# Kernel optimization log

Hardware: AMD Instinct MI355X
Metric: run time of the kernel (lower is better)

Reference implementation:

```python
import jax, jax.numpy as jnp
import numpy as np

B, L, D = 32, 128, 48          # batch, time steps, features
R = 64                          # no_reference_time_point
INIT_TIME, MAX_TS = 0.0, 48.0   # linspace bounds for reference time points


def setup_inputs() -> dict:
    key = jax.random.key(0)
    ks = jax.random.split(key, 10)
    def glorot(k, shape):
        fan_in = int(np.prod(shape[:-1])) if len(shape) > 1 else shape[0]
        fan_out = shape[-1]
        lim = float(np.sqrt(6.0 / (fan_in + fan_out)))
        return jax.random.uniform(k, shape, jnp.float32, -lim, lim)
    return {
        "X": jax.random.normal(ks[0], (B, L, D), jnp.float32),
        "T": jax.random.uniform(ks[1], (B, L, D), jnp.float32) * MAX_TS,
        "M": jax.random.uniform(ks[2], (B, L, D), jnp.float32),
        "DT": jax.random.uniform(ks[3], (B, L, D), jnp.float32),
        "P": jax.random.normal(ks[4], (B, L, D), jnp.float32),
        "alpha": glorot(ks[5], (R, 1, 1)),
        "w_t": glorot(ks[6], (R, L, D, 5)),
        "b_t": glorot(ks[7], (R, L, D, 1)),
        "w_v": glorot(ks[8], (R, L, D)),
        "b_v": glorot(ks[9], (R, 1, D)),
    }


def reference(X, T, M, DT, P, alpha, w_t, b_t, w_v, b_v) -> jnp.ndarray:
    # reference time points: [R,1,1]
    ref = jnp.linspace(INIT_TIME, MAX_TS, R, dtype=jnp.float32).reshape(R, 1, 1)
    # broadcast inputs over reference axis: [B,R,L,D]
    t = T[:, None, :, :]
    dist = jnp.abs(t - ref)                         # type_distance == 'abs'
    kernel = jnp.exp(-jax.nn.relu(alpha) * dist)    # [B,R,L,D]
    x = X[:, None, :, :] * jnp.ones((1, R, 1, 1), jnp.float32)
    intensity = jax.nn.relu(x * kernel)             # [B,R,L,D]
    # stack the 5 channels: [B,R,L,D,5]
    c = jnp.stack(
        [x,
         intensity,
         jnp.broadcast_to(M[:, None, :, :], x.shape),
         jnp.broadcast_to(DT[:, None, :, :], x.shape),
         jnp.broadcast_to(P[:, None, :, :], x.shape)],
        axis=-1)
    # temporal projection: sum over channel axis (b_t broadcast over the 5 channels)
    h = jax.nn.relu(jnp.sum(w_t * c + b_t, axis=-1))       # [B,R,L,D]
    # value projection: sum over time-step axis L (b_v [R,1,D] broadcast over L)
    out = jax.nn.relu(jnp.sum(w_v * h + b_v, axis=2))       # [B,R,D]
    return out
```

## Files before the change

### kernel.cpp

```cpp
#include <hip/hip_runtime.h>
#include <hip/hip_bf16.h>

#define PB 32
#define PL 128
#define PD 48
#define PR 64

__global__ __launch_bounds__(192) void alnn_kernel(
    const float* __restrict__ X,
    const float* __restrict__ T,
    const float* __restrict__ M,
    const float* __restrict__ DT,
    const float* __restrict__ P,
    const float* __restrict__ alpha,
    const float* __restrict__ w_t,
    const float* __restrict__ b_t,
    const float* __restrict__ w_v,
    const float* __restrict__ b_v,
    float* __restrict__ out)
{
    const int bid = blockIdx.x;
    const int r = bid & (PR - 1);
    const int b = bid >> 6;
    const int tid = threadIdx.x;
    const int lg = tid / 12;
    const int dq = tid - lg * 12;

    __shared__ float4 part[16][12];

    float ar = alpha[r];
    ar = ar > 0.0f ? ar : 0.0f;
    const float refr = 48.0f * (float)r / 63.0f;

    const int in_base = b * (PL * PD) + dq * 4;
    const int wt_base = r * (PL * PD * 5) + dq * 20;
    const int rv_base = r * (PL * PD) + dq * 4;

    float acc[4] = {0.0f, 0.0f, 0.0f, 0.0f};

    #pragma unroll
    for (int li = 0; li < 8; ++li) {
        const int l = li * 16 + lg;
        const int io = in_base + l * PD;
        const float4 x4  = *(const float4*)(X  + io);
        const float4 t4  = *(const float4*)(T  + io);
        const float4 m4  = *(const float4*)(M  + io);
        const float4 dt4 = *(const float4*)(DT + io);
        const float4 p4  = *(const float4*)(P  + io);

        const float* wp = w_t + wt_base + l * (PD * 5);
        float w[20];
        *(float4*)(w +  0) = *(const float4*)(wp +  0);
        *(float4*)(w +  4) = *(const float4*)(wp +  4);
        *(float4*)(w +  8) = *(const float4*)(wp +  8);
        *(float4*)(w + 12) = *(const float4*)(wp + 12);
        *(float4*)(w + 16) = *(const float4*)(wp + 16);

        const int vo = rv_base + l * PD;
        const float4 bt4 = *(const float4*)(b_t + vo);
        const float4 wv4 = *(const float4*)(w_v + vo);

        const float xs[4]  = {x4.x,  x4.y,  x4.z,  x4.w};
        const float ts[4]  = {t4.x,  t4.y,  t4.z,  t4.w};
        const float ms[4]  = {m4.x,  m4.y,  m4.z,  m4.w};
        const float dts[4] = {dt4.x, dt4.y, dt4.z, dt4.w};
        const float ps[4]  = {p4.x,  p4.y,  p4.z,  p4.w};
        const float bts[4] = {bt4.x, bt4.y, bt4.z, bt4.w};
        const float wvs[4] = {wv4.x, wv4.y, wv4.z, wv4.w};

        #pragma unroll
        for (int j = 0; j < 4; ++j) {
            const float x = xs[j];
            const float dist = fabsf(ts[j] - refr);
            const float kern = __expf(-ar * dist);
            float inten = x * kern;
            inten = inten > 0.0f ? inten : 0.0f;
            float h = w[j*5 + 0] * x
                    + w[j*5 + 1] * inten
                    + w[j*5 + 2] * ms[j]
                    + w[j*5 + 3] * dts[j]
                    + w[j*5 + 4] * ps[j]
                    + 5.0f * bts[j];
            h = h > 0.0f ? h : 0.0f;
            acc[j] += wvs[j] * h;
        }
    }

    part[lg][dq] = make_float4(acc[0], acc[1], acc[2], acc[3]);
    __syncthreads();

    if (tid < 12) {
        float4 s = part[0][tid];
        #pragma unroll
        for (int g = 1; g < 16; ++g) {
            const float4 q = part[g][tid];
            s.x += q.x; s.y += q.y; s.z += q.z; s.w += q.w;
        }
        const float4 bv4 = *(const float4*)(b_v + r * PD + tid * 4);
        s.x = fmaxf(s.x + 128.0f * bv4.x, 0.0f);
        s.y = fmaxf(s.y + 128.0f * bv4.y, 0.0f);
        s.z = fmaxf(s.z + 128.0f * bv4.z, 0.0f);
        s.w = fmaxf(s.w + 128.0f * bv4.w, 0.0f);
        *(float4*)(out + b * (PR * PD) + r * PD + tid * 4) = s;
    }
}

extern "C" void kernel_launch(void* const* d_in, const int* in_sizes, int n_in,
                              void* d_out, int out_size, void* d_ws, size_t ws_size,
                              hipStream_t stream) {
    const float* X     = (const float*)d_in[0];
    const float* T     = (const float*)d_in[1];
    const float* M     = (const float*)d_in[2];
    const float* DT    = (const float*)d_in[3];
    const float* P     = (const float*)d_in[4];
    const float* alpha = (const float*)d_in[5];
    const float* w_t   = (const float*)d_in[6];
    const float* b_t   = (const float*)d_in[7];
    const float* w_v   = (const float*)d_in[8];
    const float* b_v   = (const float*)d_in[9];
    float* out = (float*)d_out;

    alnn_kernel<<<PB * PR, 192, 0, stream>>>(X, T, M, DT, P, alpha, w_t, b_t, w_v, b_v, out);
}
```

Before: 109.0 us.

## Register-tile two batches by two reference points per block for weight/input reuse

Each block now computes a 2x2 tile of (batch, reference-point) pairs instead of one, so every loaded weight row is reused for two batches and every loaded input row for two reference points. This cuts global and L2 traffic per output and shrinks the grid from 2048 to 512 blocks. The cost is higher register pressure, a partial unroll of the L loop, a larger shared-memory reduction buffer, and fewer blocks to fill the GPU's compute units.

```diff
diff --git a/kernel.cpp b/kernel.cpp
--- a/kernel.cpp
+++ b/kernel.cpp
@@ -5,6 +5,38 @@
 #define PL 128
 #define PD 48
 #define PR 64
+
+__device__ __forceinline__ void compute4(
+    const float4 x4, const float4 t4, const float4 m4, const float4 dt4,
+    const float4 p4, const float* __restrict__ w20, const float4 bt4,
+    const float4 wv4, const float ar, const float refr, float4& acc)
+{
+    const float xs[4]  = {x4.x,  x4.y,  x4.z,  x4.w};
+    const float ts[4]  = {t4.x,  t4.y,  t4.z,  t4.w};
+    const float ms[4]  = {m4.x,  m4.y,  m4.z,  m4.w};
+    const float dts[4] = {dt4.x, dt4.y, dt4.z, dt4.w};
+    const float ps[4]  = {p4.x,  p4.y,  p4.z,  p4.w};
+    const float bts[4] = {bt4.x, bt4.y, bt4.z, bt4.w};
+    const float wvs[4] = {wv4.x, wv4.y, wv4.z, wv4.w};
+    float a[4] = {acc.x, acc.y, acc.z, acc.w};
+    #pragma unroll
+    for (int j = 0; j < 4; ++j) {
+        const float x = xs[j];
+        const float dist = fabsf(ts[j] - refr);
+        const float kern = __expf(-ar * dist);
+        float inten = x * kern;
+        inten = inten > 0.0f ? inten : 0.0f;
+        float h = w20[j*5 + 0] * x
+                + w20[j*5 + 1] * inten
+                + w20[j*5 + 2] * ms[j]
+                + w20[j*5 + 3] * dts[j]
+                + w20[j*5 + 4] * ps[j]
+                + 5.0f * bts[j];
+        h = h > 0.0f ? h : 0.0f;
+        a[j] += wvs[j] * h;
+    }
+    acc = make_float4(a[0], a[1], a[2], a[3]);
+}
 
 __global__ __launch_bounds__(192) void alnn_kernel(
     const float* __restrict__ X,
@@ -20,88 +52,90 @@
     float* __restrict__ out)
 {
     const int bid = blockIdx.x;
-    const int r = bid & (PR - 1);
-    const int b = bid >> 6;
+    const int rrb = bid & 31;
+    const int bbb = bid >> 5;
+    const int r0 = rrb * 2;
+    const int b0 = bbb * 2;
     const int tid = threadIdx.x;
     const int lg = tid / 12;
     const int dq = tid - lg * 12;
 
-    __shared__ float4 part[16][12];
+    __shared__ float4 part[16][49];
 
-    float ar = alpha[r];
-    ar = ar > 0.0f ? ar : 0.0f;
-    const float refr = 48.0f * (float)r / 63.0f;
+    const float ar0 = fmaxf(alpha[r0], 0.0f);
+    const float ar1 = fmaxf(alpha[r0 + 1], 0.0f);
+    const float refr0 = 48.0f * (float)r0 / 63.0f;
+    const float refr1 = 48.0f * (float)(r0 + 1) / 63.0f;
 
-    const int in_base = b * (PL * PD) + dq * 4;
-    const int wt_base = r * (PL * PD * 5) + dq * 20;
-    const int rv_base = r * (PL * PD) + dq * 4;
+    int io = b0 * (PL * PD) + lg * PD + dq * 4;
+    int wo = r0 * (PL * PD * 5) + lg * (PD * 5) + dq * 20;
+    int vo = r0 * (PL * PD) + lg * PD + dq * 4;
 
-    float acc[4] = {0.0f, 0.0f, 0.0f, 0.0f};
+    float4 acc00 = make_float4(0.f, 0.f, 0.f, 0.f);
+    float4 acc01 = make_float4(0.f, 0.f, 0.f, 0.f);
+    float4 acc10 = make_float4(0.f, 0.f, 0.f, 0.f);
+    float4 acc11 = make_float4(0.f, 0.f, 0.f, 0.f);
 
-    #pragma unroll
+    #pragma unroll 2
     for (int li = 0; li < 8; ++li) {
-        const int l = li * 16 + lg;
-        const int io = in_base + l * PD;
-        const float4 x4  = *(const float4*)(X  + io);
-        const float4 t4  = *(const float4*)(T  + io);
-        const float4 m4  = *(const float4*)(M  + io);
-        const float4 dt4 = *(const float4*)(DT + io);
-        const float4 p4  = *(const float4*)(P  + io);
+        const float4 x0  = *(const float4*)(X  + io);
+        const float4 t0  = *(const float4*)(T  + io);
+        const float4 m0  = *(const float4*)(M  + io);
+        const float4 dt0 = *(const float4*)(DT + io);
+        const float4 p0  = *(const float4*)(P  + io);
+        const float4 x1  = *(const float4*)(X  + io + PL * PD);
+        const float4 t1  = *(const float4*)(T  + io + PL * PD);
+        const float4 m1  = *(const float4*)(M  + io + PL * PD);
+        const float4 dt1 = *(const float4*)(DT + io + PL * PD);
+        const float4 p1  = *(const float4*)(P  + io + PL * PD);
 
-        const float* wp = w_t + wt_base + l * (PD * 5);
-        float w[20];
-        *(float4*)(w +  0) = *(const float4*)(wp +  0);
-        *(float4*)(w +  4) = *(const float4*)(wp +  4);
-        *(float4*)(w +  8) = *(const float4*)(wp +  8);
-        *(float4*)(w + 12) = *(const float4*)(wp + 12);
-        *(float4*)(w + 16) = *(const float4*)(wp + 16);
+        float w0[20], w1[20];
+        #pragma unroll
+        for (int q = 0; q < 5; ++q) {
+            *(float4*)(w0 + q * 4) = *(const float4*)(w_t + wo + q * 4);
+            *(float4*)(w1 + q * 4) = *(const float4*)(w_t + wo + PL * PD * 5 + q * 4);
+        }
 
-        const int vo = rv_base + l * PD;
-        const float4 bt4 = *(const float4*)(b_t + vo);
-        const float4 wv4 = *(const float4*)(w_v + vo);
+        const float4 bt0 = *(const float4*)(b_t + vo);
+        const float4 wv0 = *(const float4*)(w_v + vo);
+        const float4 bt1 = *(const float4*)(b_t + vo + PL * PD);
+        const float4 wv1 = *(const float4*)(w_v + vo + PL * PD);
 
-        const float xs[4]  = {x4.x,  x4.y,  x4.z,  x4.w};
-        const float ts[4]  = {t4.x,  t4.y,  t4.z,  t4.w};
-        const float ms[4]  = {m4.x,  m4.y,  m4.z,  m4.w};
-        const float dts[4] = {dt4.x, dt4.y, dt4.z, dt4.w};
-        const float ps[4]  = {p4.x,  p4.y,  p4.z,  p4.w};
-        const float bts[4] = {bt4.x, bt4.y, bt4.z, bt4.w};
-        const float wvs[4] = {wv4.x, wv4.y, wv4.z, wv4.w};
+        compute4(x0, t0, m0, dt0, p0, w0, bt0, wv0, ar0, refr0, acc00);
+        compute4(x0, t0, m0, dt0, p0, w1, bt1, wv1, ar1, refr1, acc01);
+        compute4(x1, t1, m1, dt1, p1, w0, bt0, wv0, ar0, refr0, acc10);
+        compute4(x1, t1, m1, dt1, p1, w1, bt1, wv1, ar1, refr1, acc11);
 
-        #pragma unroll
-        for (int j = 0; j < 4; ++j) {
-            const float x = xs[j];
-            const float dist = fabsf(ts[j] - refr);
-            const float kern = __expf(-ar * dist);
-            float inten = x * kern;
-            inten = inten > 0.0f ? inten : 0.0f;
-            float h = w[j*5 + 0] * x
-                    + w[j*5 + 1] * inten
-                    + w[j*5 + 2] * ms[j]
-                    + w[j*5 + 3] * dts[j]
-                    + w[j*5 + 4] * ps[j]
-                    + 5.0f * bts[j];
-            h = h > 0.0f ? h : 0.0f;
-            acc[j] += wvs[j] * h;
-        }
+        io += 16 * PD;
+        wo += 16 * PD * 5;
+        vo += 16 * PD;
     }
 
-    part[lg][dq] = make_float4(acc[0], acc[1], acc[2], acc[3]);
+    part[lg][ 0 + dq] = acc00;
+    part[lg][12 + dq] = acc01;
+    part[lg][24 + dq] = acc10;
+    part[lg][36 + dq] = acc11;
     __syncthreads();
 
-    if (tid < 12) {
-        float4 s = part[0][tid];
+    if (tid < 48) {
+        const int o = tid;
+        const int bi = o / 24;
+        const int ri = (o - bi * 24) / 12;
+        const int dqo = o - bi * 24 - ri * 12;
+        float4 s = part[0][o];
         #pragma unroll
         for (int g = 1; g < 16; ++g) {
-            const float4 q = part[g][tid];
+            const float4 q = part[g][o];
             s.x += q.x; s.y += q.y; s.z += q.z; s.w += q.w;
         }
-        const float4 bv4 = *(const float4*)(b_v + r * PD + tid * 4);
+        const int r = r0 + ri;
+        const int b = b0 + bi;
+        const float4 bv4 = *(const float4*)(b_v + r * PD + dqo * 4);
         s.x = fmaxf(s.x + 128.0f * bv4.x, 0.0f);
         s.y = fmaxf(s.y + 128.0f * bv4.y, 0.0f);
         s.z = fmaxf(s.z + 128.0f * bv4.z, 0.0f);
         s.w = fmaxf(s.w + 128.0f * bv4.w, 0.0f);
-        *(float4*)(out + b * (PR * PD) + r * PD + tid * 4) = s;
+        *(float4*)(out + b * (PR * PD) + r * PD + dqo * 4) = s;
     }
 }
 
@@ -120,5 +154,5 @@
     const float* b_v   = (const float*)d_in[9];
     float* out = (float*)d_out;
 
-    alnn_kernel<<<PB * PR, 192, 0, stream>>>(X, T, M, DT, P, alpha, w_t, b_t, w_v, b_v, out);
+    alnn_kernel<<<512, 192, 0, stream>>>(X, T, M, DT, P, alpha, w_t, b_t, w_v, b_v, out);
 }
```

Result: faster. 101.2 us (-7.2%).
